# Optimization experiments

Hardware: AMD Instinct MI355X
Metric: run time of the kernel (lower is better)

The kernel has to match this reference:

```python
import jax, jax.numpy as jnp
import numpy as np

N, D, K = 32768, 256, 4096


def setup_inputs() -> dict:
    key = jax.random.key(0)
    k1, k2 = jax.random.split(key)
    x = jax.random.normal(k1, (N, D), dtype=jnp.float32)
    codebook = jax.random.normal(k2, (K, D), dtype=jnp.float32)
    return {"x": x, "codebook": codebook}


def reference(x, codebook):
    """Euclidean VQ forward: cdist -> argmin -> gather, with straight-through output
    and commitment loss, matching the module's assign_pass math
    (d2 = x2 + c2 - 2 x@C^T, clamped at 0, argmin over codes).
    """
    # squared L2 distances [N, K], single fused expression (no double softmax-style passes)
    x2 = jnp.sum(x * x, axis=-1, keepdims=True)          # [N, 1]
    c2 = jnp.sum(codebook * codebook, axis=-1)           # [K]
    d2 = jnp.maximum(x2 + c2[None, :] - 2.0 * (x @ codebook.T), 0.0)  # [N, K]
    ind = jnp.argmin(d2, axis=-1)                        # [N] int cluster assignment
    quantize = jnp.take(codebook, ind, axis=0)           # [N, D] gather
    # commitment loss: ||sg(q) - x||^2 mean
    commit_loss = jnp.mean(jnp.square(jax.lax.stop_gradient(quantize) - x))
    # straight-through estimator: forward value = quantize, grad passes to x
    out = x + jax.lax.stop_gradient(quantize - x)
    return out, ind, commit_loss
```

## Files before the change

kernel.cpp:

```cpp
#include <hip/hip_runtime.h>
#include <hip/hip_bf16.h>

#define VQ_N 32768
#define VQ_D 256
#define VQ_K 4096
#define BAND 16.0f
#define QCAP (2u * 1024u * 1024u)
#define BUFCAP 2048

typedef __attribute__((ext_vector_type(8))) short short8;
typedef __attribute__((ext_vector_type(4))) float f32x4;

__device__ __forceinline__ unsigned fmap(float f) {
    unsigned b = __float_as_uint(f);
    return (b & 0x80000000u) ? ~b : (b | 0x80000000u);
}
__device__ __forceinline__ float fmapinv(unsigned u) {
    unsigned b = (u & 0x80000000u) ? (u & 0x7FFFFFFFu) : ~u;
    return __uint_as_float(b);
}

__device__ __forceinline__ void async16(const void* g, void* l) {
    __builtin_amdgcn_global_load_lds(
        (const __attribute__((address_space(1))) unsigned int*)g,
        (__attribute__((address_space(3))) unsigned int*)l, 16, 0, 0);
}

__device__ __forceinline__ short8 pack8(float4 a, float4 b) {
    union { __hip_bfloat16 h[8]; short8 s8; } u;
    u.h[0] = __float2bfloat16(a.x); u.h[1] = __float2bfloat16(a.y);
    u.h[2] = __float2bfloat16(a.z); u.h[3] = __float2bfloat16(a.w);
    u.h[4] = __float2bfloat16(b.x); u.h[5] = __float2bfloat16(b.y);
    u.h[6] = __float2bfloat16(b.z); u.h[7] = __float2bfloat16(b.w);
    return u.s8;
}

__global__ __launch_bounds__(256)
void prep_all_kernel(const float* __restrict__ x, const float* __restrict__ cb,
                     short8* __restrict__ xb_sw, short8* __restrict__ cbb_sw,
                     float* __restrict__ c2, unsigned int* __restrict__ rowmin,
                     unsigned long long* __restrict__ keys,
                     unsigned int* __restrict__ ctrl ) {
    const int b = blockIdx.x, t = threadIdx.x;
    if (b < 2048) {
        #pragma unroll
        for (int h = 0; h < 2; ++h) {
            const int u   = t + h * 256;
            const int row = b * 16 + (u >> 5);
            const int s   = u & 31;
            const int q   = s ^ (row & 15);
            const float4 a = reinterpret_cast<const float4*>(x)[(size_t)row * 64 + q * 2];
            const float4 c = reinterpret_cast<const float4*>(x)[(size_t)row * 64 + q * 2 + 1];
            xb_sw[(size_t)row * 32 + s] = pack8(a, c);
        }
    } else if (b < 2304) {
        const int code = (b - 2048) * 16 + (t >> 4);
        float ss = 0.0f;
        #pragma unroll
        for (int h = 0; h < 2; ++h) {
            const int j  = (t & 15) * 2 + h;
            const int ks = j >> 2, sl = j & 3;
            const int kq = (sl - (code >> 1)) & 3;
            const int k  = ks * 32 + kq * 8;
            const float4 a = reinterpret_cast<const float4*>(cb)[(size_t)code * 64 + k / 4];
            const float4 c = reinterpret_cast<const float4*>(cb)[(size_t)code * 64 + k / 4 + 1];
            ss += a.x*a.x + a.y*a.y + a.z*a.z + a.w*a.w
                + c.x*c.x + c.y*c.y + c.z*c.z + c.w*c.w;
            const float4 na = make_float4(-2.f*a.x, -2.f*a.y, -2.f*a.z, -2.f*a.w);
            const float4 nc = make_float4(-2.f*c.x, -2.f*c.y, -2.f*c.z, -2.f*c.w);
            cbb_sw[(size_t)code * 32 + j] = pack8(na, nc);
        }
        #pragma unroll
        for (int off = 1; off < 16; off <<= 1) ss += __shfl_xor(ss, off, 64);
        if ((t & 15) == 0) c2[code] = ss;
    } else if (b < 2432) {
        const int i = (b - 2304) * 256 + t;
        rowmin[i] = 0xFFFFFFFFu;
        keys[i]   = ~0ull;
    } else {
        if (t < 8) ctrl[t] = 0u;
    }
}

template<bool COLLECT>
__global__ __launch_bounds__(512, 2)
void sweep_kernel(const short8* __restrict__ xb_sw,
                  const short8* __restrict__ cbb_sw,
                  const float* __restrict__ c2,
                  unsigned int* __restrict__ rowmin,
                  unsigned int* __restrict__ qcnt,
                  unsigned int* __restrict__ overflow,
                  unsigned int* __restrict__ queue) {
    __shared__ __attribute__((aligned(16))) char As[128 * 512];
    __shared__ __attribute__((aligned(16))) char Bs[2][256 * 64];
    __shared__ unsigned int rowmin_s[128];
    __shared__ float        thr_s[128];
    __shared__ unsigned int qbuf[BUFCAP];
    __shared__ int qn_s, qbase_s;

    const int t = threadIdx.x;
    const int lane = t & 63, wave = t >> 6;
    const int wr = wave >> 2, wc = wave & 3;
    const int fr = lane & 15, kg = lane >> 4;
    const int rowbase = blockIdx.x * 128;
    const int code0   = blockIdx.y * 1024;

    if (COLLECT) {
        if (t < 128) thr_s[t] = fmapinv(rowmin[rowbase + t]) + BAND;
        if (t == 0) qn_s = 0;
    } else {
        if (t < 128) rowmin_s[t] = 0xFFFFFFFFu;
    }

    {
        const char* asrc = (const char*)xb_sw + (size_t)rowbase * 512 + wave * 8192
                           + lane * 16;
        char* adst = As + wave * 8192;
        #pragma unroll
        for (int i = 0; i < 8; ++i)
            async16(asrc + i * 1024, adst + i * 1024);
    }
    {
        const int cg0 = code0;
        #pragma unroll
        for (int i = 0; i < 2; ++i) {
            const int code = cg0 + wave * 32 + i * 16 + (lane >> 2);
            async16((const char*)cbb_sw + (size_t)code * 512 + (lane & 3) * 16,
                    Bs[0] + wave * 2048 + i * 1024);
        }
    }
    __syncthreads();

    float runv[4][4];
    #pragma unroll
    for (int m = 0; m < 4; ++m)
        #pragma unroll
        for (int r = 0; r < 4; ++r) runv[m][r] = 3.4e38f;

    f32x4 acc[4][4];
    #pragma unroll
    for (int m = 0; m < 4; ++m)
        #pragma unroll
        for (int n = 0; n < 4; ++n) acc[m][n] = (f32x4){0.f, 0.f, 0.f, 0.f};

    int cur = 0;
    for (int step = 0; step < 32; ++step) {
        if (step + 1 < 32) {
            const int ncct = (step + 1) >> 3, nks = (step + 1) & 7;
            const int cg = code0 + ncct * 256;
            #pragma unroll
            for (int i = 0; i < 2; ++i) {
                const int code = cg + wave * 32 + i * 16 + (lane >> 2);
                async16((const char*)cbb_sw + (size_t)code * 512 + nks * 64
                            + (lane & 3) * 16,
                        Bs[cur ^ 1] + wave * 2048 + i * 1024);
            }
        }
        const int ks = step & 7;

        short8 af[4], bf[4];
        #pragma unroll
        for (int m = 0; m < 4; ++m) {
            const int row = wr * 64 + m * 16 + fr;
            const int s   = ((ks << 2) | kg) ^ fr;
            af[m] = *reinterpret_cast<const short8*>(&As[row * 512 + (s << 4)]);
        }
        #pragma unroll
        for (int n = 0; n < 4; ++n) {
            const int c = wc * 64 + n * 16 + fr;
            const int s = (kg + (c >> 1)) & 3;
            bf[n] = *reinterpret_cast<const short8*>(&Bs[cur][c * 64 + (s << 4)]);
        }
        #pragma unroll
        for (int m = 0; m < 4; ++m)
            #pragma unroll
            for (int n = 0; n < 4; ++n)
                acc[m][n] = __builtin_amdgcn_mfma_f32_16x16x32_bf16(af[m], bf[n], acc[m][n], 0, 0, 0);

        __syncthreads();
        cur ^= 1;

        if (ks == 7) {
            const int cct = step >> 3;
            float c2v[4];
            #pragma unroll
            for (int n = 0; n < 4; ++n)
                c2v[n] = c2[code0 + cct * 256 + wc * 64 + n * 16 + fr];
            #pragma unroll
            for (int m = 0; m < 4; ++m) {
                #pragma unroll
                for (int r = 0; r < 4; ++r) {
                    if (COLLECT) {
                        const int lrow = wr * 64 + m * 16 + kg * 4 + r;
                        const float thr = thr_s[lrow];
                        #pragma unroll
                        for (int n = 0; n < 4; ++n) {
                            const float v = acc[m][n][r] + c2v[n];
                            if (v <= thr) {
                                const int code = code0 + cct * 256 + wc * 64 + n * 16 + fr;
                                const int pos = atomicAdd(&qn_s, 1);
                                if (pos < BUFCAP)
                                    qbuf[pos] = ((unsigned)(rowbase + lrow) << 12) | (unsigned)code;
                            }
                        }
                    } else {
                        float v = acc[m][0][r] + c2v[0];
                        #pragma unroll
                        for (int n = 1; n < 4; ++n) v = fminf(v, acc[m][n][r] + c2v[n]);
                        runv[m][r] = fminf(runv[m][r], v);
                    }
                }
            }
            #pragma unroll
            for (int m = 0; m < 4; ++m)
                #pragma unroll
                for (int n = 0; n < 4; ++n) acc[m][n] = (f32x4){0.f, 0.f, 0.f, 0.f};
        }
    }

    if (COLLECT) {
        __syncthreads();
        if (t == 0) {
            int n = qn_s;
            if (n > BUFCAP) { atomicOr(overflow, 1u); n = BUFCAP; }
            qbase_s = (int)atomicAdd(qcnt, (unsigned)n);
            qn_s = n;
        }
        __syncthreads();
        const unsigned base = (unsigned)qbase_s;
        for (int i = t; i < qn_s; i += 512) {
            const unsigned p = base + (unsigned)i;
            if (p < QCAP) queue[p] = qbuf[i];
        }
    } else {
        #pragma unroll
        for (int m = 0; m < 4; ++m)
            #pragma unroll
            for (int r = 0; r < 4; ++r) {
                float v = runv[m][r];
                #pragma unroll
                for (int off = 1; off < 16; off <<= 1)
                    v = fminf(v, __shfl_xor(v, off, 64));
                if (fr == 0)
                    atomicMin(&rowmin_s[wr * 64 + m * 16 + kg * 4 + r], fmap(v));
            }
        __syncthreads();
        if (t < 128) atomicMin(&rowmin[rowbase + t], rowmin_s[t]);
    }
}

__global__ __launch_bounds__(256)
void qrerank_kernel(const float* __restrict__ x, const float* __restrict__ cb,
                    const float* __restrict__ c2,
                    const unsigned int* __restrict__ qcnt,
                    const unsigned int* __restrict__ overflow,
                    const unsigned int* __restrict__ queue,
                    unsigned long long* __restrict__ keys) {
    const int t = threadIdx.x;
    const int g  = t >> 4;
    const int sl = t & 15;
    const unsigned raw = *qcnt;
    const unsigned total = raw > QCAP ? QCAP : raw;
    const unsigned stride = gridDim.x * 16;
    for (unsigned e = blockIdx.x * 16 + g; e < total; e += stride) {
        const unsigned ent = queue[e];
        const int row = (int)(ent >> 12);
        const int code = (int)(ent & 0xFFFu);
        float d = 0.0f;
        #pragma unroll
        for (int i = 0; i < 4; ++i) {
            const float4 xv = reinterpret_cast<const float4*>(x)[(size_t)row * 64 + i * 16 + sl];
            const float4 cv = reinterpret_cast<const float4*>(cb)[(size_t)code * 64 + i * 16 + sl];
            d += xv.x * cv.x + xv.y * cv.y + xv.z * cv.z + xv.w * cv.w;
        }
        #pragma unroll
        for (int off = 1; off < 16; off <<= 1) d += __shfl_xor(d, off, 64);
        const float s = fmaf(-2.0f, d, c2[code]);
        if (sl == 0)
            atomicMin(&keys[row],
                      ((unsigned long long)fmap(s) << 32) | (unsigned)code);
    }
    if (raw > QCAP || *overflow) {
        const int wave = t >> 6, lane = t & 63;
        for (int row = blockIdx.x * 4 + wave; row < VQ_N; row += gridDim.x * 4) {
            const float4 xv = reinterpret_cast<const float4*>(x)[(size_t)row * 64 + lane];
            float bv = 3.4e38f; int bk = 0;
            for (int k = 0; k < VQ_K; ++k) {
                const float4 cv = reinterpret_cast<const float4*>(cb)[(size_t)k * 64 + lane];
                float d = fmaf(xv.x, cv.x, fmaf(xv.y, cv.y, fmaf(xv.z, cv.z, xv.w * cv.w)));
                #pragma unroll
                for (int off = 1; off < 64; off <<= 1) d += __shfl_xor(d, off, 64);
                const float s = fmaf(-2.0f, d, c2[k]);
                if (s < bv) { bv = s; bk = k; }
            }
            if (lane == 0)
                atomicMin(&keys[row],
                          ((unsigned long long)fmap(bv) << 32) | (unsigned)bk);
        }
    }
}

__global__ __launch_bounds__(256)
void finalize_kernel(const float* __restrict__ x, const float* __restrict__ cb,
                     const unsigned long long* __restrict__ keys,
                     float* __restrict__ out, float* __restrict__ ind_out,
                     float* __restrict__ partials) {
    const int wave = threadIdx.x >> 6, lane = threadIdx.x & 63;
    const int row = blockIdx.x * 4 + wave;
    const int code = (int)(keys[row] & 0xFFFFFFFFull);
    const float4 qv = reinterpret_cast<const float4*>(cb)[(size_t)code * 64 + lane];
    const float4 xv = reinterpret_cast<const float4*>(x)[(size_t)row * 64 + lane];
    reinterpret_cast<float4*>(out)[(size_t)row * 64 + lane] = qv;
    if (lane == 0) ind_out[row] = (float)code;
    const float dx = qv.x - xv.x, dy = qv.y - xv.y, dz = qv.z - xv.z, dw = qv.w - xv.w;
    float s = dx * dx + dy * dy + dz * dz + dw * dw;
    #pragma unroll
    for (int off = 1; off < 64; off <<= 1) s += __shfl_xor(s, off, 64);
    __shared__ float ls[4];
    if (lane == 0) ls[wave] = s;
    __syncthreads();
    if (threadIdx.x == 0) partials[blockIdx.x] = ls[0] + ls[1] + ls[2] + ls[3];
}

__global__ __launch_bounds__(256)
void loss_reduce_kernel(const float* __restrict__ partials,
                        float* __restrict__ loss_out) {
    const int wave = threadIdx.x >> 6, lane = threadIdx.x & 63;
    float s = 0.0f;
    for (int i = threadIdx.x; i < VQ_N / 4; i += 256) s += partials[i];
    #pragma unroll
    for (int off = 1; off < 64; off <<= 1) s += __shfl_xor(s, off, 64);
    __shared__ float ls[4];
    if (lane == 0) ls[wave] = s;
    __syncthreads();
    if (threadIdx.x == 0)
        *loss_out = (ls[0] + ls[1] + ls[2] + ls[3])
                    * (1.0f / ((float)VQ_N * (float)VQ_D));
}

extern "C" void kernel_launch(void* const* d_in, const int* in_sizes, int n_in,
                              void* d_out, int out_size, void* d_ws, size_t ws_size,
                              hipStream_t stream) {
    const float* x  = (const float*)d_in[0];
    const float* cb = (const float*)d_in[1];
    float* out      = (float*)d_out;
    float* ind_out  = out + (size_t)VQ_N * VQ_D;
    float* loss_out = ind_out + VQ_N;

    char* w = (char*)d_ws;
    float*              c2     = (float*)w;
    unsigned int*       rowmin = (unsigned int*)(w + 16384);
    unsigned long long* keys   = (unsigned long long*)(w + 147456);
    unsigned int*       ctrl   = (unsigned int*)(w + 409600);
    unsigned int*       qcnt     = ctrl + 0;
    unsigned int*       overflow = ctrl + 1;
    short8*             cbb_sw = (short8*)(w + 409664);
    float*              partials = (float*)rowmin;

    short8*       xb_sw = (short8*)d_out;
    unsigned int* queue = (unsigned int*)((char*)d_out + (16u << 20));

    prep_all_kernel<<<2433, 256, 0, stream>>>(x, cb, xb_sw, cbb_sw, c2,
                                              rowmin, keys, ctrl);

    dim3 gs(VQ_N / 128, 4);
    sweep_kernel<false><<<gs, 512, 0, stream>>>(xb_sw, cbb_sw, c2, rowmin,
                                                qcnt, overflow, queue);
    sweep_kernel<true ><<<gs, 512, 0, stream>>>(xb_sw, cbb_sw, c2, rowmin,
                                                qcnt, overflow, queue);

    qrerank_kernel<<<1024, 256, 0, stream>>>(x, cb, c2, qcnt, overflow, queue, keys);

    finalize_kernel<<<VQ_N / 4, 256, 0, stream>>>(x, cb, keys, out, ind_out,
                                                  partials);
    loss_reduce_kernel<<<1, 256, 0, stream>>>(partials, loss_out);
}
```

Baseline: 362.0 us.

## Merge two-pass sweep into a single pass with running-min candidate collection

Replaces the separate min-finding sweep and candidate-collection sweep with one sweep. Each block now walks all 4096 codes, updates a per-row running minimum in shared memory after every 256-code tile, and queues codes that fall within the band of that running minimum. This halves the bf16 MFMA distance work and removes one kernel launch along with the global rowmin traffic. In exchange the grid shrinks from 1024 to 256 blocks, and each tile now carries an extra barrier. Because early tiles compare against a looser prefix minimum, more candidates are queued, so the shared-memory buffer is doubled and the rerank grid is doubled to handle them.

```diff
diff --git a/kernel.cpp b/kernel.cpp
--- a/kernel.cpp
+++ b/kernel.cpp
@@ -6,7 +6,7 @@
 #define VQ_K 4096
 #define BAND 16.0f
 #define QCAP (2u * 1024u * 1024u)
-#define BUFCAP 2048
+#define BUFCAP 4096
 
 typedef __attribute__((ext_vector_type(8))) short short8;
 typedef __attribute__((ext_vector_type(4))) float f32x4;
@@ -38,7 +38,7 @@
 __global__ __launch_bounds__(256)
 void prep_all_kernel(const float* __restrict__ x, const float* __restrict__ cb,
                      short8* __restrict__ xb_sw, short8* __restrict__ cbb_sw,
-                     float* __restrict__ c2, unsigned int* __restrict__ rowmin,
+                     float* __restrict__ c2,
                      unsigned long long* __restrict__ keys,
                      unsigned int* __restrict__ ctrl ) {
     const int b = blockIdx.x, t = threadIdx.x;
@@ -74,27 +74,22 @@
         for (int off = 1; off < 16; off <<= 1) ss += __shfl_xor(ss, off, 64);
         if ((t & 15) == 0) c2[code] = ss;
     } else if (b < 2432) {
-        const int i = (b - 2304) * 256 + t;
-        rowmin[i] = 0xFFFFFFFFu;
-        keys[i]   = ~0ull;
+        keys[(b - 2304) * 256 + t] = ~0ull;
     } else {
         if (t < 8) ctrl[t] = 0u;
     }
 }
 
-template<bool COLLECT>
 __global__ __launch_bounds__(512, 2)
 void sweep_kernel(const short8* __restrict__ xb_sw,
                   const short8* __restrict__ cbb_sw,
                   const float* __restrict__ c2,
-                  unsigned int* __restrict__ rowmin,
                   unsigned int* __restrict__ qcnt,
                   unsigned int* __restrict__ overflow,
                   unsigned int* __restrict__ queue) {
     __shared__ __attribute__((aligned(16))) char As[128 * 512];
     __shared__ __attribute__((aligned(16))) char Bs[2][256 * 64];
     __shared__ unsigned int rowmin_s[128];
-    __shared__ float        thr_s[128];
     __shared__ unsigned int qbuf[BUFCAP];
     __shared__ int qn_s, qbase_s;
 
@@ -103,14 +98,9 @@
     const int wr = wave >> 2, wc = wave & 3;
     const int fr = lane & 15, kg = lane >> 4;
     const int rowbase = blockIdx.x * 128;
-    const int code0   = blockIdx.y * 1024;
-
-    if (COLLECT) {
-        if (t < 128) thr_s[t] = fmapinv(rowmin[rowbase + t]) + BAND;
-        if (t == 0) qn_s = 0;
-    } else {
-        if (t < 128) rowmin_s[t] = 0xFFFFFFFFu;
-    }
+
+    if (t < 128) rowmin_s[t] = 0xFFFFFFFFu;
+    if (t == 0) qn_s = 0;
 
     {
         const char* asrc = (const char*)xb_sw + (size_t)rowbase * 512 + wave * 8192
@@ -120,22 +110,13 @@
         for (int i = 0; i < 8; ++i)
             async16(asrc + i * 1024, adst + i * 1024);
     }
-    {
-        const int cg0 = code0;
-        #pragma unroll
-        for (int i = 0; i < 2; ++i) {
-            const int code = cg0 + wave * 32 + i * 16 + (lane >> 2);
-            async16((const char*)cbb_sw + (size_t)code * 512 + (lane & 3) * 16,
-                    Bs[0] + wave * 2048 + i * 1024);
-        }
-    }
-    __syncthreads();
-
-    float runv[4][4];
     #pragma unroll
-    for (int m = 0; m < 4; ++m)
-        #pragma unroll
-        for (int r = 0; r < 4; ++r) runv[m][r] = 3.4e38f;
+    for (int i = 0; i < 2; ++i) {
+        const int code = wave * 32 + i * 16 + (lane >> 2);
+        async16((const char*)cbb_sw + (size_t)code * 512 + (lane & 3) * 16,
+                Bs[0] + wave * 2048 + i * 1024);
+    }
+    __syncthreads();
 
     f32x4 acc[4][4];
     #pragma unroll
@@ -144,13 +125,12 @@
         for (int n = 0; n < 4; ++n) acc[m][n] = (f32x4){0.f, 0.f, 0.f, 0.f};
 
     int cur = 0;
-    for (int step = 0; step < 32; ++step) {
-        if (step + 1 < 32) {
+    for (int step = 0; step < 128; ++step) {
+        if (step + 1 < 128) {
             const int ncct = (step + 1) >> 3, nks = (step + 1) & 7;
-            const int cg = code0 + ncct * 256;
             #pragma unroll
             for (int i = 0; i < 2; ++i) {
-                const int code = cg + wave * 32 + i * 16 + (lane >> 2);
+                const int code = ncct * 256 + wave * 32 + i * 16 + (lane >> 2);
                 async16((const char*)cbb_sw + (size_t)code * 512 + nks * 64
                             + (lane & 3) * 16,
                         Bs[cur ^ 1] + wave * 2048 + i * 1024);
@@ -185,29 +165,39 @@
             float c2v[4];
             #pragma unroll
             for (int n = 0; n < 4; ++n)
-                c2v[n] = c2[code0 + cct * 256 + wc * 64 + n * 16 + fr];
+                c2v[n] = c2[cct * 256 + wc * 64 + n * 16 + fr];
+
             #pragma unroll
             for (int m = 0; m < 4; ++m) {
                 #pragma unroll
                 for (int r = 0; r < 4; ++r) {
-                    if (COLLECT) {
-                        const int lrow = wr * 64 + m * 16 + kg * 4 + r;
-                        const float thr = thr_s[lrow];
-                        #pragma unroll
-                        for (int n = 0; n < 4; ++n) {
-                            const float v = acc[m][n][r] + c2v[n];
-                            if (v <= thr) {
-                                const int code = code0 + cct * 256 + wc * 64 + n * 16 + fr;
-                                const int pos = atomicAdd(&qn_s, 1);
-                                if (pos < BUFCAP)
-                                    qbuf[pos] = ((unsigned)(rowbase + lrow) << 12) | (unsigned)code;
-                            }
+                    float v = acc[m][0][r] + c2v[0];
+                    #pragma unroll
+                    for (int n = 1; n < 4; ++n) v = fminf(v, acc[m][n][r] + c2v[n]);
+                    #pragma unroll
+                    for (int off = 1; off < 16; off <<= 1)
+                        v = fminf(v, __shfl_xor(v, off, 64));
+                    if (fr == 0)
+                        atomicMin(&rowmin_s[wr * 64 + m * 16 + kg * 4 + r], fmap(v));
+                }
+            }
+            __syncthreads();
+
+            #pragma unroll
+            for (int m = 0; m < 4; ++m) {
+                #pragma unroll
+                for (int r = 0; r < 4; ++r) {
+                    const int lrow = wr * 64 + m * 16 + kg * 4 + r;
+                    const float thr = fmapinv(rowmin_s[lrow]) + BAND;
+                    #pragma unroll
+                    for (int n = 0; n < 4; ++n) {
+                        const float v = acc[m][n][r] + c2v[n];
+                        if (v <= thr) {
+                            const int code = cct * 256 + wc * 64 + n * 16 + fr;
+                            const int pos = atomicAdd(&qn_s, 1);
+                            if (pos < BUFCAP)
+                                qbuf[pos] = ((unsigned)(rowbase + lrow) << 12) | (unsigned)code;
                         }
-                    } else {
-                        float v = acc[m][0][r] + c2v[0];
-                        #pragma unroll
-                        for (int n = 1; n < 4; ++n) v = fminf(v, acc[m][n][r] + c2v[n]);
-                        runv[m][r] = fminf(runv[m][r], v);
                     }
                 }
             }
@@ -218,34 +208,18 @@
         }
     }
 
-    if (COLLECT) {
-        __syncthreads();
-        if (t == 0) {
-            int n = qn_s;
-            if (n > BUFCAP) { atomicOr(overflow, 1u); n = BUFCAP; }
-            qbase_s = (int)atomicAdd(qcnt, (unsigned)n);
-            qn_s = n;
-        }
-        __syncthreads();
-        const unsigned base = (unsigned)qbase_s;
-        for (int i = t; i < qn_s; i += 512) {
-            const unsigned p = base + (unsigned)i;
-            if (p < QCAP) queue[p] = qbuf[i];
-        }
-    } else {
-        #pragma unroll
-        for (int m = 0; m < 4; ++m)
-            #pragma unroll
-            for (int r = 0; r < 4; ++r) {
-                float v = runv[m][r];
-                #pragma unroll
-                for (int off = 1; off < 16; off <<= 1)
-                    v = fminf(v, __shfl_xor(v, off, 64));
-                if (fr == 0)
-                    atomicMin(&rowmin_s[wr * 64 + m * 16 + kg * 4 + r], fmap(v));
-            }
-        __syncthreads();
-        if (t < 128) atomicMin(&rowmin[rowbase + t], rowmin_s[t]);
+    __syncthreads();
+    if (t == 0) {
+        int n = qn_s;
+        if (n > BUFCAP) { atomicOr(overflow, 1u); n = BUFCAP; }
+        qbase_s = (int)atomicAdd(qcnt, (unsigned)n);
+        qn_s = n;
+    }
+    __syncthreads();
+    const unsigned base = (unsigned)qbase_s;
+    for (int i = t; i < qn_s; i += 512) {
+        const unsigned p = base + (unsigned)i;
+        if (p < QCAP) queue[p] = qbuf[i];
     }
 }
 
@@ -348,28 +322,24 @@
     float* loss_out = ind_out + VQ_N;
 
     char* w = (char*)d_ws;
-    float*              c2     = (float*)w;
-    unsigned int*       rowmin = (unsigned int*)(w + 16384);
-    unsigned long long* keys   = (unsigned long long*)(w + 147456);
-    unsigned int*       ctrl   = (unsigned int*)(w + 409600);
+    float*              c2       = (float*)w;
+    float*              partials = (float*)(w + 16384);
+    unsigned long long* keys     = (unsigned long long*)(w + 147456);
+    unsigned int*       ctrl     = (unsigned int*)(w + 409600);
     unsigned int*       qcnt     = ctrl + 0;
     unsigned int*       overflow = ctrl + 1;
-    short8*             cbb_sw = (short8*)(w + 409664);
-    float*              partials = (float*)rowmin;
+    short8*             cbb_sw   = (short8*)(w + 409664);
 
     short8*       xb_sw = (short8*)d_out;
     unsigned int* queue = (unsigned int*)((char*)d_out + (16u << 20));
 
     prep_all_kernel<<<2433, 256, 0, stream>>>(x, cb, xb_sw, cbb_sw, c2,
-                                              rowmin, keys, ctrl);
-
-    dim3 gs(VQ_N / 128, 4);
-    sweep_kernel<false><<<gs, 512, 0, stream>>>(xb_sw, cbb_sw, c2, rowmin,
-                                                qcnt, overflow, queue);
-    sweep_kernel<true ><<<gs, 512, 0, stream>>>(xb_sw, cbb_sw, c2, rowmin,
-                                                qcnt, overflow, queue);
-
-    qrerank_kernel<<<1024, 256, 0, stream>>>(x, cb, c2, qcnt, overflow, queue, keys);
+                                              keys, ctrl);
+
+    sweep_kernel<<<VQ_N / 128, 512, 0, stream>>>(xb_sw, cbb_sw, c2,
+                                                 qcnt, overflow, queue);
+
+    qrerank_kernel<<<2048, 256, 0, stream>>>(x, cb, c2, qcnt, overflow, queue, keys);
 
     finalize_kernel<<<VQ_N / 4, 256, 0, stream>>>(x, cb, keys, out, ind_out,
                                                   partials);
```

Measured after the change: 345.2 us. 4.6% less time.
